# Kernel optimization log

Measured on AMD Instinct MI355X. Metric: run time of the kernel, lower is better.

Reference implementation:

```python
import jax, jax.numpy as jnp
import numpy as np

B, F0, K = 256, 40, 32          # batch, num fields, embedding dim
CIN_SIZE = [200, 200]            # layer widths (field_num[1:])


def setup_inputs() -> dict:
    key = jax.random.key(0)
    ks = jax.random.split(key, 1 + 4 * len(CIN_SIZE))
    field_num = [F0] + CIN_SIZE
    d = {"inputs": jax.random.normal(ks[0], (B, F0, K), dtype=jnp.float32)}
    for i in range(len(CIN_SIZE)):
        # W_query: (1, Fi, K); W_key/W_value: (1, F0, K); cin_W: (1, F0*Fi, F_{i+1})
        d[f"wq{i}"] = jax.random.normal(ks[1 + 4 * i], (1, field_num[i], K), dtype=jnp.float32) * 0.05
        d[f"wk{i}"] = jax.random.normal(ks[2 + 4 * i], (1, F0, K), dtype=jnp.float32) * 0.05
        d[f"wv{i}"] = jax.random.normal(ks[3 + 4 * i], (1, F0, K), dtype=jnp.float32) * 0.05
        lim = (6.0 / (F0 * field_num[i] + field_num[i + 1])) ** 0.5  # glorot uniform
        d[f"cw{i}"] = jax.random.uniform(ks[4 + 4 * i], (1, F0 * field_num[i], field_num[i + 1]),
                                         minval=-lim, maxval=lim, dtype=jnp.float32)
    return d


def _cin(inputs, params):
    # inputs: [B, F0, K]; params: list of (wq, wk, wv, cw) per CIN layer
    Bb, F0_, Kk = inputs.shape
    res = inputs
    outs = []
    for (wq, wk, wv, cw) in params:
        x0_wk = inputs * wk                 # [B, F0, K]
        x0_wv = inputs * wv                 # [B, F0, K]
        xi_wq = res * wq                    # [B, Fi, K]
        # per-embedding-slot outer product scores: phi[b,k,f0,fi]
        phi = jnp.einsum('bfk,bgk->bkfg', x0_wk, xi_wq)
        # exp + normalize over F0 axis == softmax over axis=2
        alpha = jax.nn.softmax(phi, axis=2)                      # [B, K, F0, Fi]
        x = alpha * jnp.transpose(x0_wv, (0, 2, 1))[:, :, :, None]  # [B, K, F0, Fi]
        x = x.reshape(Bb, Kk, -1)           # flatten (f0, fi) row-major -> f0*Fi + fi
        # conv1d with kernel width 1 == channel matmul: [B, K, F0*Fi] @ [F0*Fi, F_{i+1}]
        out = jnp.einsum('bkc,cj->bjk', x, cw[0])                # [B, F_{i+1}, K]
        outs.append(out)
        res = out
    cat = jnp.concatenate(outs, axis=1)     # [B, sum(cin_size), K]
    return cat.sum(axis=-1)                 # [B, sum(cin_size)]


def reference(inputs, wq0, wk0, wv0, cw0, wq1, wk1, wv1, cw1):
    return _cin(inputs, [(wq0, wk0, wv0, cw0), (wq1, wk1, wv1, cw1)])
```

## Files before the change

### kernel.cpp

```cpp
#include <hip/hip_runtime.h>
#include <hip/hip_bf16.h>


#define NF0  40
#define KD   32
#define NJ   200
#define NTHR 512

typedef short bf16x8 __attribute__((ext_vector_type(8)));
typedef float f32x16 __attribute__((ext_vector_type(16)));
typedef unsigned short u16;
typedef unsigned int   u32;
typedef unsigned long long u64;

static __device__ __forceinline__ u16 f2bf(float f) {
    __hip_bfloat16 h = __float2bfloat16(f);
    return *reinterpret_cast<u16*>(&h);
}
static __device__ __forceinline__ float bf2f(u16 u) {
    u32 x = ((u32)u) << 16;
    float f;
    __builtin_memcpy(&f, &x, 4);
    return f;
}

template<int FI>
__global__ __launch_bounds__(256)
void pack_b(const float* __restrict__ cw, u16* __restrict__ bp, int G) {
    __shared__ u16 s[160][33];
    const int fi0 = blockIdx.x * 4;
    const int nt  = blockIdx.y;
    const int t   = threadIdx.x;
    #pragma unroll
    for (int it = 0; it < 5; ++it) {
        int idx = it * 256 + t;
        int rl = idx >> 3, q4 = idx & 7;
        int f0 = rl >> 2, fl = rl & 3;
        int fi = fi0 + fl;
        int j0 = nt * 32 + q4 * 4;
        float4 v = make_float4(0.f, 0.f, 0.f, 0.f);
        if (fi < FI && j0 <= NJ - 4)
            v = *reinterpret_cast<const float4*>(cw + (size_t)(f0 * FI + fi) * NJ + j0);
        int cl = fl * 40 + f0;
        s[cl][q4 * 4 + 0] = f2bf(v.x);
        s[cl][q4 * 4 + 1] = f2bf(v.y);
        s[cl][q4 * 4 + 2] = f2bf(v.z);
        s[cl][q4 * 4 + 3] = f2bf(v.w);
    }
    __syncthreads();
    for (int ft = t; ft < 640; ft += 256) {
        int g = ft >> 6, l = ft & 63;
        u16 v[8];
        #pragma unroll
        for (int i = 0; i < 8; ++i) v[i] = s[g * 16 + 8 * (l >> 5) + i][l & 31];
        *reinterpret_cast<bf16x8*>(bp + ((size_t)(nt * G + blockIdx.x * 10 + g) * 64 + l) * 8)
            = *reinterpret_cast<const bf16x8*>(v);
    }
}

__global__ __launch_bounds__(NTHR, 4)
void cin_layer0(const float* __restrict__ x0,
                const float* __restrict__ wq, const float* __restrict__ wk,
                const float* __restrict__ wv,
                const u16* __restrict__ bp, u16* __restrict__ resp) {
    __shared__ float s_xk[1280], s_xv[1280], s_q[640];
    __shared__ u64 s_XT[32 * 48];
    const int tid = threadIdx.x;
    const int b = blockIdx.x >> 1, half = blockIdx.x & 1;
    const int wid = tid >> 6, lane = tid & 63;
    const int jcol = lane & 31, hh = lane >> 5;

    for (int i = tid; i < 1280; i += NTHR) {
        float v = x0[(size_t)b * 1280 + i];
        s_xk[i] = v * wk[i];
        s_xv[i] = v * wv[i];
    }
    for (int i = tid; i < 640; i += NTHR) {
        int fi = half * 20 + (i >> 5), k = i & 31;
        s_q[i] = x0[(size_t)b * 1280 + fi * 32 + k] * wq[fi * 32 + k];
    }
    __syncthreads();

    const int sk = lane & 31, sh = lane >> 5, sfil = wid;
    float xkr[20], xvr[20];
    if (wid < 4) {
        #pragma unroll
        for (int i = 0; i < 20; ++i) {
            xkr[i] = s_xk[(sh * 20 + i) * 32 + sk];
            xvr[i] = s_xv[(sh * 20 + i) * 32 + sk];
        }
    }

    f32x16 acc;
    #pragma unroll
    for (int r = 0; r < 16; ++r) acc[r] = 0.f;
    const int nt = wid;
    char* aptr = (char*)s_XT + jcol * 384;
    const int aswz = (jcol & 7) << 4;

    for (int ch = 0; ch < 5; ++ch) {
        if (wid < 4) {
            const float q = s_q[(ch * 4 + sfil) * 32 + sk];
            float e[20], d = 0.f;
            #pragma unroll
            for (int i = 0; i < 20; ++i) { e[i] = __expf(xkr[i] * q); d += e[i]; }
            d += __shfl_xor(d, 32);
            const float rr = 1.0f / d;
            char* rb = (char*)s_XT + sk * 384;
            const int swz = (sk & 7) << 4;
            #pragma unroll
            for (int p = 0; p < 5; ++p) {
                u64 w = (u64)f2bf(e[4*p+0] * rr * xvr[4*p+0])
                      | ((u64)f2bf(e[4*p+1] * rr * xvr[4*p+1]) << 16)
                      | ((u64)f2bf(e[4*p+2] * rr * xvr[4*p+2]) << 32)
                      | ((u64)f2bf(e[4*p+3] * rr * xvr[4*p+3]) << 48);
                *reinterpret_cast<u64*>(rb + ((sfil * 80 + sh * 40 + p * 8) ^ swz)) = w;
            }
        }
        __syncthreads();
        __builtin_amdgcn_s_setprio(1);
        if (wid < 7) {
            #pragma unroll
            for (int ks = 0; ks < 10; ++ks) {
                bf16x8 a = *reinterpret_cast<const bf16x8*>(aptr + ((ks * 32 + hh * 16) ^ aswz));
                const int g = half * 50 + ch * 10 + ks;
                bf16x8 bf = *reinterpret_cast<const bf16x8*>(
                    bp + ((size_t)(nt * 100 + g) * 64 + lane) * 8);
                acc = __builtin_amdgcn_mfma_f32_32x32x16_bf16(a, bf, acc, 0, 0, 0);
            }
        }
        __builtin_amdgcn_s_setprio(0);
        __syncthreads();
    }

    if (wid < 7) {
        const int j = nt * 32 + jcol;
        if (j < NJ) {
            u16* dst = resp + (size_t)(half * 256 + b) * 6400 + j * 32;
            #pragma unroll
            for (int rg = 0; rg < 4; ++rg) {
                u64 w = (u64)f2bf(acc[4*rg+0]) | ((u64)f2bf(acc[4*rg+1]) << 16)
                      | ((u64)f2bf(acc[4*rg+2]) << 32) | ((u64)f2bf(acc[4*rg+3]) << 48);
                *reinterpret_cast<u64*>(dst + 8 * rg + 4 * hh) = w;
            }
        }
    }
}

__global__ __launch_bounds__(NTHR, 4)
void cin_layer1(const float* __restrict__ x0, const u16* __restrict__ resp,
                const float* __restrict__ wq, const float* __restrict__ wk,
                const float* __restrict__ wv,
                const u16* __restrict__ bp, float* __restrict__ out) {
    __shared__ float s_xk[2560], s_xv[2560], s_q[3328];
    __shared__ u64 s_XT[64 * 48];
    const int tid = threadIdx.x;
    const int bg = blockIdx.x >> 2, split = blockIdx.x & 3;
    const int b0 = bg * 2;
    const int wid = tid >> 6, lane = tid & 63;

    if (split == 0) {
        for (int idx = tid; idx < 2 * NJ; idx += NTHR) {
            const int bb = idx / NJ, j = idx - bb * NJ;
            const u16* r0 = resp + (size_t)(b0 + bb) * 6400 + j * 32;
            const u16* r1 = resp + (size_t)(256 + b0 + bb) * 6400 + j * 32;
            float s = 0.f;
            #pragma unroll
            for (int q8 = 0; q8 < 4; ++q8) {
                bf16x8 v0 = *reinterpret_cast<const bf16x8*>(r0 + q8 * 8);
                bf16x8 v1 = *reinterpret_cast<const bf16x8*>(r1 + q8 * 8);
                #pragma unroll
                for (int i = 0; i < 8; ++i) s += bf2f((u16)v0[i]) + bf2f((u16)v1[i]);
            }
            out[(size_t)(b0 + bb) * 400 + j] = s;
        }
    }

    for (int idx = tid; idx < 2560; idx += NTHR) {
        const int bb = idx / 1280, r = idx - bb * 1280;
        float v = x0[(size_t)(b0 + bb) * 1280 + r];
        s_xk[idx] = v * wk[r];
        s_xv[idx] = v * wv[r];
    }
    for (int idx = tid; idx < 3328; idx += NTHR) {
        const int bb = idx / 1664, rr = idx - bb * 1664;
        const int fi = split * 52 + (rr >> 5), k = rr & 31;
        float qv = 0.f;
        if (fi < 200) {
            float rv = bf2f(resp[(size_t)(b0 + bb) * 6400 + fi * 32 + k])
                     + bf2f(resp[(size_t)(256 + b0 + bb) * 6400 + fi * 32 + k]);
            qv = rv * wq[fi * 32 + k];
        }
        s_q[idx] = qv;
    }
    __syncthreads();

    const int sbb = wid >> 2, sfil = wid & 3, sh = lane >> 5, sk = lane & 31;
    const int srow = sbb * 32 + sk;
    float xkr[20], xvr[20];
    #pragma unroll
    for (int i = 0; i < 20; ++i) {
        xkr[i] = s_xk[sbb * 1280 + (sh * 20 + i) * 32 + sk];
        xvr[i] = s_xv[sbb * 1280 + (sh * 20 + i) * 32 + sk];
    }
    char* srb = (char*)s_XT + srow * 384;
    const int sswz = (srow & 7) << 4;

    const int mg = wid & 1, ng = wid >> 1;
    const int nt0 = ng, nt1 = ng + 4;
    const int ntc = (ng < 3) ? 2 : 1;
    f32x16 acc[2];
    #pragma unroll
    for (int t = 0; t < 2; ++t)
        #pragma unroll
        for (int r = 0; r < 16; ++r) acc[t][r] = 0.f;
    const int arow = mg * 32 + (lane & 31);
    char* aptr = (char*)s_XT + arow * 384;
    const int aswz = (arow & 7) << 4;
    const int ah = (lane >> 5) * 16;

    for (int ch = 0; ch < 13; ++ch) {
        const int fig = split * 52 + ch * 4 + sfil;
        if (fig < 200) {
            const float q = s_q[sbb * 1664 + (ch * 4 + sfil) * 32 + sk];
            float e[20], d = 0.f;
            #pragma unroll
            for (int i = 0; i < 20; ++i) { e[i] = __expf(xkr[i] * q); d += e[i]; }
            d += __shfl_xor(d, 32);
            const float rr = 1.0f / d;
            #pragma unroll
            for (int p = 0; p < 5; ++p) {
                u64 w = (u64)f2bf(e[4*p+0] * rr * xvr[4*p+0])
                      | ((u64)f2bf(e[4*p+1] * rr * xvr[4*p+1]) << 16)
                      | ((u64)f2bf(e[4*p+2] * rr * xvr[4*p+2]) << 32)
                      | ((u64)f2bf(e[4*p+3] * rr * xvr[4*p+3]) << 48);
                *reinterpret_cast<u64*>(srb + ((sfil * 80 + sh * 40 + p * 8) ^ sswz)) = w;
            }
        } else {
            #pragma unroll
            for (int p = 0; p < 5; ++p)
                *reinterpret_cast<u64*>(srb + ((sfil * 80 + sh * 40 + p * 8) ^ sswz)) = 0ull;
        }
        __syncthreads();
        __builtin_amdgcn_s_setprio(1);
        #pragma unroll
        for (int ks = 0; ks < 10; ++ks) {
            bf16x8 a = *reinterpret_cast<const bf16x8*>(aptr + ((ks * 32 + ah) ^ aswz));
            const int g = split * 130 + ch * 10 + ks;
            bf16x8 bf0 = *reinterpret_cast<const bf16x8*>(
                bp + ((size_t)(nt0 * 520 + g) * 64 + lane) * 8);
            acc[0] = __builtin_amdgcn_mfma_f32_32x32x16_bf16(a, bf0, acc[0], 0, 0, 0);
            if (ntc == 2) {
                bf16x8 bf1 = *reinterpret_cast<const bf16x8*>(
                    bp + ((size_t)(nt1 * 520 + g) * 64 + lane) * 8);
                acc[1] = __builtin_amdgcn_mfma_f32_32x32x16_bf16(a, bf1, acc[1], 0, 0, 0);
            }
        }
        __builtin_amdgcn_s_setprio(0);
        __syncthreads();
    }

    #pragma unroll
    for (int t = 0; t < 2; ++t) {
        if (t < ntc) {
            float s = 0.f;
            #pragma unroll
            for (int r = 0; r < 16; ++r) s += acc[t][r];
            s += __shfl_xor(s, 32);
            const int nt = (t == 0) ? nt0 : nt1;
            const int j = nt * 32 + (lane & 31);
            if (lane < 32 && j < NJ)
                atomicAdd(&out[(size_t)(b0 + mg) * 400 + 200 + j], s);
        }
    }
}

extern "C" void kernel_launch(void* const* d_in, const int* in_sizes, int n_in,
                              void* d_out, int out_size, void* d_ws, size_t ws_size,
                              hipStream_t stream) {
    const float* x0  = (const float*)d_in[0];
    const float* wq0 = (const float*)d_in[1];
    const float* wk0 = (const float*)d_in[2];
    const float* wv0 = (const float*)d_in[3];
    const float* cw0 = (const float*)d_in[4];
    const float* wq1 = (const float*)d_in[5];
    const float* wk1 = (const float*)d_in[6];
    const float* wv1 = (const float*)d_in[7];
    const float* cw1 = (const float*)d_in[8];
    float* out = (float*)d_out;

    char* ws = (char*)d_ws;
    u16* resp = (u16*)ws;
    u16* bp0  = (u16*)(ws + 6553600);
    u16* bp1  = (u16*)(ws + 6553600 + 716800);

    hipMemsetAsync(d_out, 0, (size_t)out_size * 4, stream);

    pack_b<40> <<<dim3(10, 7), 256, 0, stream>>>(cw0, bp0, 100);
    pack_b<200><<<dim3(52, 7), 256, 0, stream>>>(cw1, bp1, 520);

    cin_layer0<<<512, NTHR, 0, stream>>>(x0, wq0, wk0, wv0, bp0, resp);
    cin_layer1<<<512, NTHR, 0, stream>>>(x0, resp, wq1, wk1, wv1, bp1, out);
}
```

Before: 187.6 us.

## Double-buffer softmax tiles and merge layer0 half-splits into one block per batch

Both CIN layer kernels now double-buffer the shared-memory A tile: the softmax for the next chunk is computed and stored while the MFMA loop consumes the current chunk, which drops one barrier per iteration. Layer0 now runs one block per batch row covering all 40 fi, using all 8 waves for softmax. That removes the partial-result split and the extra resp summation in layer1. The xk/xv staging through shared memory is replaced by direct global loads into registers. In exchange, layer0 launches half as many blocks and its occupancy bound drops to 2, which may reduce latency hiding.

Result: slower. 202.9 us (+8.2%).

```diff
diff --git a/kernel.cpp b/kernel.cpp
--- a/kernel.cpp
+++ b/kernel.cpp
@@ -58,194 +58,200 @@
     }
 }
 
-__global__ __launch_bounds__(NTHR, 4)
+__global__ __launch_bounds__(NTHR, 2)
 void cin_layer0(const float* __restrict__ x0,
                 const float* __restrict__ wq, const float* __restrict__ wk,
                 const float* __restrict__ wv,
                 const u16* __restrict__ bp, u16* __restrict__ resp) {
-    __shared__ float s_xk[1280], s_xv[1280], s_q[640];
-    __shared__ u64 s_XT[32 * 48];
+    __shared__ float s_q[1280];
+    __shared__ u64 s_XT[2][32 * 96];
+
     const int tid = threadIdx.x;
-    const int b = blockIdx.x >> 1, half = blockIdx.x & 1;
+    const int b = blockIdx.x;
     const int wid = tid >> 6, lane = tid & 63;
-    const int jcol = lane & 31, hh = lane >> 5;
-
-    for (int i = tid; i < 1280; i += NTHR) {
-        float v = x0[(size_t)b * 1280 + i];
-        s_xk[i] = v * wk[i];
-        s_xv[i] = v * wv[i];
-    }
-    for (int i = tid; i < 640; i += NTHR) {
-        int fi = half * 20 + (i >> 5), k = i & 31;
-        s_q[i] = x0[(size_t)b * 1280 + fi * 32 + k] * wq[fi * 32 + k];
-    }
-    __syncthreads();
-
-    const int sk = lane & 31, sh = lane >> 5, sfil = wid;
+    const int sfil = wid, sh = lane >> 5, sk = lane & 31;
+
+    for (int i = tid; i < 1280; i += NTHR)
+        s_q[i] = x0[(size_t)b * 1280 + i] * wq[i];
+
     float xkr[20], xvr[20];
-    if (wid < 4) {
-        #pragma unroll
-        for (int i = 0; i < 20; ++i) {
-            xkr[i] = s_xk[(sh * 20 + i) * 32 + sk];
-            xvr[i] = s_xv[(sh * 20 + i) * 32 + sk];
-        }
-    }
+    #pragma unroll
+    for (int i = 0; i < 20; ++i) {
+        const int off = (sh * 20 + i) * 32 + sk;
+        const float v = x0[(size_t)b * 1280 + off];
+        xkr[i] = v * wk[off];
+        xvr[i] = v * wv[off];
+    }
+
+    const int soff = sfil * 80 + sh * 40;
+    const int sswz = (sk & 7) << 4;
+    char* srb0 = (char*)s_XT[0] + sk * 768;
+    char* srb1 = (char*)s_XT[1] + sk * 768;
+
+    const int nt = wid;
+    const int arow = lane & 31;
+    const int aswz = (arow & 7) << 4;
+    char* apb0 = (char*)s_XT[0] + arow * 768;
+    char* apb1 = (char*)s_XT[1] + arow * 768;
+    const int ah = (lane >> 5) * 16;
 
     f32x16 acc;
     #pragma unroll
     for (int r = 0; r < 16; ++r) acc[r] = 0.f;
-    const int nt = wid;
-    char* aptr = (char*)s_XT + jcol * 384;
-    const int aswz = (jcol & 7) << 4;
+
+    auto softmax_store = [&](char* rb, int ch) {
+        const float q = s_q[(ch * 8 + sfil) * 32 + sk];
+        float e[20], d = 0.f;
+        #pragma unroll
+        for (int i = 0; i < 20; ++i) { e[i] = __expf(xkr[i] * q); d += e[i]; }
+        d += __shfl_xor(d, 32);
+        const float rr = 1.0f / d;
+        #pragma unroll
+        for (int p = 0; p < 5; ++p) {
+            u64 w = (u64)f2bf(e[4*p+0] * rr * xvr[4*p+0])
+                  | ((u64)f2bf(e[4*p+1] * rr * xvr[4*p+1]) << 16)
+                  | ((u64)f2bf(e[4*p+2] * rr * xvr[4*p+2]) << 32)
+                  | ((u64)f2bf(e[4*p+3] * rr * xvr[4*p+3]) << 48);
+            *reinterpret_cast<u64*>(rb + ((soff + p * 8) ^ sswz)) = w;
+        }
+    };
+
+    __syncthreads();
+    softmax_store(srb0, 0);
+    __syncthreads();
 
     for (int ch = 0; ch < 5; ++ch) {
-        if (wid < 4) {
-            const float q = s_q[(ch * 4 + sfil) * 32 + sk];
+        if (ch + 1 < 5) softmax_store((ch & 1) ? srb0 : srb1, ch + 1);
+        if (wid < 7) {
+            char* apb = (ch & 1) ? apb1 : apb0;
+            #pragma unroll
+            for (int ks = 0; ks < 20; ++ks) {
+                bf16x8 a = *reinterpret_cast<const bf16x8*>(apb + ((ks * 32 + ah) ^ aswz));
+                const int g = ch * 20 + ks;
+                bf16x8 bf = *reinterpret_cast<const bf16x8*>(
+                    bp + ((size_t)(nt * 100 + g) * 64 + lane) * 8);
+                acc = __builtin_amdgcn_mfma_f32_32x32x16_bf16(a, bf, acc, 0, 0, 0);
+            }
+        }
+        __syncthreads();
+    }
+
+    if (wid < 7) {
+        const int j = nt * 32 + (lane & 31);
+        if (j < NJ) {
+            u16* dst = resp + (size_t)b * 6400 + j * 32;
+            #pragma unroll
+            for (int rg = 0; rg < 4; ++rg) {
+                u64 w = (u64)f2bf(acc[4*rg+0]) | ((u64)f2bf(acc[4*rg+1]) << 16)
+                      | ((u64)f2bf(acc[4*rg+2]) << 32) | ((u64)f2bf(acc[4*rg+3]) << 48);
+                *reinterpret_cast<u64*>(dst + 8 * rg + 4 * (lane >> 5)) = w;
+            }
+        }
+    }
+}
+
+__global__ __launch_bounds__(NTHR, 4)
+void cin_layer1(const float* __restrict__ x0, const u16* __restrict__ resp,
+                const float* __restrict__ wq, const float* __restrict__ wk,
+                const float* __restrict__ wv,
+                const u16* __restrict__ bp, float* __restrict__ out) {
+    __shared__ float s_q[3328];
+    __shared__ u64 s_XT[2][64 * 48];
+
+    const int tid = threadIdx.x;
+    const int bg = blockIdx.x >> 2, split = blockIdx.x & 3;
+    const int b0 = bg * 2;
+    const int wid = tid >> 6, lane = tid & 63;
+
+    if (split == 0) {
+        for (int idx = tid; idx < 2 * NJ; idx += NTHR) {
+            const int bb = idx / NJ, j = idx - bb * NJ;
+            const u16* rp = resp + (size_t)(b0 + bb) * 6400 + j * 32;
+            float s = 0.f;
+            #pragma unroll
+            for (int q8 = 0; q8 < 4; ++q8) {
+                bf16x8 v = *reinterpret_cast<const bf16x8*>(rp + q8 * 8);
+                #pragma unroll
+                for (int i = 0; i < 8; ++i) s += bf2f((u16)v[i]);
+            }
+            out[(size_t)(b0 + bb) * 400 + j] = s;
+        }
+    }
+
+    for (int idx = tid; idx < 3328; idx += NTHR) {
+        const int bb = idx / 1664, rr = idx - bb * 1664;
+        const int fi = split * 52 + (rr >> 5), k = rr & 31;
+        float qv = 0.f;
+        if (fi < 200)
+            qv = bf2f(resp[(size_t)(b0 + bb) * 6400 + fi * 32 + k]) * wq[fi * 32 + k];
+        s_q[idx] = qv;
+    }
+
+    const int sbb = wid >> 2, sfil = wid & 3, sh = lane >> 5, sk = lane & 31;
+    float xkr[20], xvr[20];
+    #pragma unroll
+    for (int i = 0; i < 20; ++i) {
+        const int off = (sh * 20 + i) * 32 + sk;
+        const float v = x0[(size_t)(b0 + sbb) * 1280 + off];
+        xkr[i] = v * wk[off];
+        xvr[i] = v * wv[off];
+    }
+
+    const int srow = sbb * 32 + sk;
+    const int soff = sfil * 80 + sh * 40;
+    const int sswz = (srow & 7) << 4;
+    char* srb0 = (char*)s_XT[0] + srow * 384;
+    char* srb1 = (char*)s_XT[1] + srow * 384;
+
+    const int mg = wid & 1, ng = wid >> 1;
+    const int nt0 = ng, nt1 = ng + 4;
+    const int ntc = (ng < 3) ? 2 : 1;
+    const int arow = mg * 32 + (lane & 31);
+    const int aswz = (arow & 7) << 4;
+    char* apb0 = (char*)s_XT[0] + arow * 384;
+    char* apb1 = (char*)s_XT[1] + arow * 384;
+    const int ah = (lane >> 5) * 16;
+
+    f32x16 acc[2];
+    #pragma unroll
+    for (int t = 0; t < 2; ++t)
+        #pragma unroll
+        for (int r = 0; r < 16; ++r) acc[t][r] = 0.f;
+
+    auto softmax_store = [&](char* rb, int ch) {
+        const int fig = split * 52 + ch * 4 + sfil;
+        if (fig < 200) {
+            const float q = s_q[sbb * 1664 + (ch * 4 + sfil) * 32 + sk];
             float e[20], d = 0.f;
             #pragma unroll
             for (int i = 0; i < 20; ++i) { e[i] = __expf(xkr[i] * q); d += e[i]; }
             d += __shfl_xor(d, 32);
             const float rr = 1.0f / d;
-            char* rb = (char*)s_XT + sk * 384;
-            const int swz = (sk & 7) << 4;
             #pragma unroll
             for (int p = 0; p < 5; ++p) {
                 u64 w = (u64)f2bf(e[4*p+0] * rr * xvr[4*p+0])
                       | ((u64)f2bf(e[4*p+1] * rr * xvr[4*p+1]) << 16)
                       | ((u64)f2bf(e[4*p+2] * rr * xvr[4*p+2]) << 32)
                       | ((u64)f2bf(e[4*p+3] * rr * xvr[4*p+3]) << 48);
-                *reinterpret_cast<u64*>(rb + ((sfil * 80 + sh * 40 + p * 8) ^ swz)) = w;
-            }
-        }
-        __syncthreads();
-        __builtin_amdgcn_s_setprio(1);
-        if (wid < 7) {
-            #pragma unroll
-            for (int ks = 0; ks < 10; ++ks) {
-                bf16x8 a = *reinterpret_cast<const bf16x8*>(aptr + ((ks * 32 + hh * 16) ^ aswz));
-                const int g = half * 50 + ch * 10 + ks;
-                bf16x8 bf = *reinterpret_cast<const bf16x8*>(
-                    bp + ((size_t)(nt * 100 + g) * 64 + lane) * 8);
-                acc = __builtin_amdgcn_mfma_f32_32x32x16_bf16(a, bf, acc, 0, 0, 0);
-            }
-        }
-        __builtin_amdgcn_s_setprio(0);
-        __syncthreads();
-    }
-
-    if (wid < 7) {
-        const int j = nt * 32 + jcol;
-        if (j < NJ) {
-            u16* dst = resp + (size_t)(half * 256 + b) * 6400 + j * 32;
-            #pragma unroll
-            for (int rg = 0; rg < 4; ++rg) {
-                u64 w = (u64)f2bf(acc[4*rg+0]) | ((u64)f2bf(acc[4*rg+1]) << 16)
-                      | ((u64)f2bf(acc[4*rg+2]) << 32) | ((u64)f2bf(acc[4*rg+3]) << 48);
-                *reinterpret_cast<u64*>(dst + 8 * rg + 4 * hh) = w;
-            }
-        }
-    }
-}
-
-__global__ __launch_bounds__(NTHR, 4)
-void cin_layer1(const float* __restrict__ x0, const u16* __restrict__ resp,
-                const float* __restrict__ wq, const float* __restrict__ wk,
-                const float* __restrict__ wv,
-                const u16* __restrict__ bp, float* __restrict__ out) {
-    __shared__ float s_xk[2560], s_xv[2560], s_q[3328];
-    __shared__ u64 s_XT[64 * 48];
-    const int tid = threadIdx.x;
-    const int bg = blockIdx.x >> 2, split = blockIdx.x & 3;
-    const int b0 = bg * 2;
-    const int wid = tid >> 6, lane = tid & 63;
-
-    if (split == 0) {
-        for (int idx = tid; idx < 2 * NJ; idx += NTHR) {
-            const int bb = idx / NJ, j = idx - bb * NJ;
-            const u16* r0 = resp + (size_t)(b0 + bb) * 6400 + j * 32;
-            const u16* r1 = resp + (size_t)(256 + b0 + bb) * 6400 + j * 32;
-            float s = 0.f;
-            #pragma unroll
-            for (int q8 = 0; q8 < 4; ++q8) {
-                bf16x8 v0 = *reinterpret_cast<const bf16x8*>(r0 + q8 * 8);
-                bf16x8 v1 = *reinterpret_cast<const bf16x8*>(r1 + q8 * 8);
-                #pragma unroll
-                for (int i = 0; i < 8; ++i) s += bf2f((u16)v0[i]) + bf2f((u16)v1[i]);
-            }
-            out[(size_t)(b0 + bb) * 400 + j] = s;
-        }
-    }
-
-    for (int idx = tid; idx < 2560; idx += NTHR) {
-        const int bb = idx / 1280, r = idx - bb * 1280;
-        float v = x0[(size_t)(b0 + bb) * 1280 + r];
-        s_xk[idx] = v * wk[r];
-        s_xv[idx] = v * wv[r];
-    }
-    for (int idx = tid; idx < 3328; idx += NTHR) {
-        const int bb = idx / 1664, rr = idx - bb * 1664;
-        const int fi = split * 52 + (rr >> 5), k = rr & 31;
-        float qv = 0.f;
-        if (fi < 200) {
-            float rv = bf2f(resp[(size_t)(b0 + bb) * 6400 + fi * 32 + k])
-                     + bf2f(resp[(size_t)(256 + b0 + bb) * 6400 + fi * 32 + k]);
-            qv = rv * wq[fi * 32 + k];
-        }
-        s_q[idx] = qv;
-    }
-    __syncthreads();
-
-    const int sbb = wid >> 2, sfil = wid & 3, sh = lane >> 5, sk = lane & 31;
-    const int srow = sbb * 32 + sk;
-    float xkr[20], xvr[20];
-    #pragma unroll
-    for (int i = 0; i < 20; ++i) {
-        xkr[i] = s_xk[sbb * 1280 + (sh * 20 + i) * 32 + sk];
-        xvr[i] = s_xv[sbb * 1280 + (sh * 20 + i) * 32 + sk];
-    }
-    char* srb = (char*)s_XT + srow * 384;
-    const int sswz = (srow & 7) << 4;
-
-    const int mg = wid & 1, ng = wid >> 1;
-    const int nt0 = ng, nt1 = ng + 4;
-    const int ntc = (ng < 3) ? 2 : 1;
-    f32x16 acc[2];
-    #pragma unroll
-    for (int t = 0; t < 2; ++t)
-        #pragma unroll
-        for (int r = 0; r < 16; ++r) acc[t][r] = 0.f;
-    const int arow = mg * 32 + (lane & 31);
-    char* aptr = (char*)s_XT + arow * 384;
-    const int aswz = (arow & 7) << 4;
-    const int ah = (lane >> 5) * 16;
+                *reinterpret_cast<u64*>(rb + ((soff + p * 8) ^ sswz)) = w;
+            }
+        } else {
+            #pragma unroll
+            for (int p = 0; p < 5; ++p)
+                *reinterpret_cast<u64*>(rb + ((soff + p * 8) ^ sswz)) = 0ull;
+        }
+    };
+
+    __syncthreads();
+    softmax_store(srb0, 0);
+    __syncthreads();
 
     for (int ch = 0; ch < 13; ++ch) {
-        const int fig = split * 52 + ch * 4 + sfil;
-        if (fig < 200) {
-            const float q = s_q[sbb * 1664 + (ch * 4 + sfil) * 32 + sk];
-            float e[20], d = 0.f;
-            #pragma unroll
-            for (int i = 0; i < 20; ++i) { e[i] = __expf(xkr[i] * q); d += e[i]; }
-            d += __shfl_xor(d, 32);
-            const float rr = 1.0f / d;
-            #pragma unroll
-            for (int p = 0; p < 5; ++p) {
-                u64 w = (u64)f2bf(e[4*p+0] * rr * xvr[4*p+0])
-                      | ((u64)f2bf(e[4*p+1] * rr * xvr[4*p+1]) << 16)
-                      | ((u64)f2bf(e[4*p+2] * rr * xvr[4*p+2]) << 32)
-                      | ((u64)f2bf(e[4*p+3] * rr * xvr[4*p+3]) << 48);
-                *reinterpret_cast<u64*>(srb + ((sfil * 80 + sh * 40 + p * 8) ^ sswz)) = w;
-            }
-        } else {
-            #pragma unroll
-            for (int p = 0; p < 5; ++p)
-                *reinterpret_cast<u64*>(srb + ((sfil * 80 + sh * 40 + p * 8) ^ sswz)) = 0ull;
-        }
-        __syncthreads();
-        __builtin_amdgcn_s_setprio(1);
+        if (ch + 1 < 13) softmax_store((ch & 1) ? srb0 : srb1, ch + 1);
+        char* apb = (ch & 1) ? apb1 : apb0;
         #pragma unroll
         for (int ks = 0; ks < 10; ++ks) {
-            bf16x8 a = *reinterpret_cast<const bf16x8*>(aptr + ((ks * 32 + ah) ^ aswz));
+            bf16x8 a = *reinterpret_cast<const bf16x8*>(apb + ((ks * 32 + ah) ^ aswz));
             const int g = split * 130 + ch * 10 + ks;
             bf16x8 bf0 = *reinterpret_cast<const bf16x8*>(
                 bp + ((size_t)(nt0 * 520 + g) * 64 + lane) * 8);
@@ -256,7 +262,6 @@
                 acc[1] = __builtin_amdgcn_mfma_f32_32x32x16_bf16(a, bf1, acc[1], 0, 0, 0);
             }
         }
-        __builtin_amdgcn_s_setprio(0);
         __syncthreads();
     }
 
@@ -291,14 +296,14 @@
 
     char* ws = (char*)d_ws;
     u16* resp = (u16*)ws;
-    u16* bp0  = (u16*)(ws + 6553600);
-    u16* bp1  = (u16*)(ws + 6553600 + 716800);
+    u16* bp0  = (u16*)(ws + 3276800);
+    u16* bp1  = (u16*)(ws + 3276800 + 716800);
 
     hipMemsetAsync(d_out, 0, (size_t)out_size * 4, stream);
 
     pack_b<40> <<<dim3(10, 7), 256, 0, stream>>>(cw0, bp0, 100);
     pack_b<200><<<dim3(52, 7), 256, 0, stream>>>(cw1, bp1, 520);
 
-    cin_layer0<<<512, NTHR, 0, stream>>>(x0, wq0, wk0, wv0, bp0, resp);
+    cin_layer0<<<256, NTHR, 0, stream>>>(x0, wq0, wk0, wv0, bp0, resp);
     cin_layer1<<<512, NTHR, 0, stream>>>(x0, resp, wq1, wk1, wv1, bp1, out);
 }
```
